# Kernel tuning notes

Measured on AMD Instinct MI355X. Metric: run time of the kernel, lower is better.

Reference implementation:

```python
import jax, jax.numpy as jnp
import numpy as np

START_TAG = 0
END_TAG = 63
NEG_INF = -10000.0


def setup_inputs() -> dict:
    key = jax.random.key(0)
    k1, k2, k3 = jax.random.split(key, 3)
    S, D, L = 32768, 1024, 64  # seq_len, feature_dim, num_labels
    feats = jax.random.normal(k1, (S, D), jnp.float32)
    W = jax.random.normal(k2, (L, D), jnp.float32) * 0.02  # nn.Linear weight [out,in]
    b = jnp.zeros((L,), jnp.float32)
    transitions = jax.random.normal(k3, (L, L), jnp.float32)
    transitions = transitions.at[START_TAG, :].set(NEG_INF).at[:, END_TAG].set(NEG_INF)
    return {"feats": feats, "W": W, "b": b, "transitions": transitions}


def reference(feats, W, b, transitions):
    # emissions: [S, L]
    emissions = feats @ W.T + b

    # Viterbi forward pass.  scores[j] after step t = best path score ending in label j.
    init_scores = transitions[:, START_TAG] + emissions[0]

    def step(scores, emit):
        # swt[j, i] = scores[i] + T[j, i]  (transition i -> j)
        swt = scores[None, :] + transitions  # [L, L]
        new_scores = emit + jnp.max(swt, axis=-1)
        back_ptr = jnp.argmax(swt, axis=-1)
        return new_scores, back_ptr

    final_scores, back_ptrs = jax.lax.scan(step, init_scores, emissions[1:])
    final_scores = final_scores + transitions[END_TAG]

    viterbi_score = jnp.max(final_scores)
    last_tag = jnp.argmax(final_scores)

    # Backtrack: tag[t-1] = back_ptrs[t-1][tag[t]] (back_ptrs[k] is for time k+1).
    def back(tag, bp):
        return bp[tag], tag

    first_tag, rest_tags = jax.lax.scan(back, last_tag, back_ptrs, reverse=True)
    tag_seq = jnp.concatenate([first_tag[None], rest_tags])  # [S]
    return viterbi_score, tag_seq
```

## Files before the change

kernel.cpp:

```cpp
#include <hip/hip_runtime.h>

#define S_LEN 32768
#define D_DIM 1024
#define L_LAB 64
#define LC 32
#define NCH (S_LEN / LC)
#define H_WARM 32
#define CHUNK 128
#define NCHUNK (S_LEN / CHUNK)

#define EM_OFF   0
#define SC_OFF   (S_LEN * 64 * 4)
#define BP_OFF   (SC_OFF + S_LEN * 64 * 4)
#define MAPS_OFF (BP_OFF + S_LEN * 64)
#define BND_OFF  (MAPS_OFF + NCHUNK * 64)
#define WIN_OFF  (BND_OFF + 256)
#define WBF_OFF  (WIN_OFF + NCH * 4)

typedef __attribute__((ext_vector_type(8))) short short8;
typedef __attribute__((ext_vector_type(4))) float floatx4;

__device__ inline unsigned short f32_bf16_rne(float f) {
    unsigned v = __float_as_uint(f);
    v += 0x7FFFu + ((v >> 16) & 1u);
    return (unsigned short)(v >> 16);
}

__global__ __launch_bounds__(256) void wconv_kernel(
        const float* __restrict__ W, unsigned short* __restrict__ Wbf) {
    int i = blockIdx.x * 256 + threadIdx.x;
    Wbf[i] = f32_bf16_rne(W[i]);
}

__global__ __launch_bounds__(256) __attribute__((amdgpu_waves_per_eu(2, 2)))
void emis_kernel(
        const float* __restrict__ feats, const unsigned short* __restrict__ Wbf,
        const float* __restrict__ bvec, float* __restrict__ em) {
    __shared__ __align__(16) unsigned short As[64 * 72];
    __shared__ __align__(16) unsigned short Bs[64 * 72];

    const int tid = threadIdx.x;
    const int lan = tid & 15;
    const int q   = (tid >> 4) & 3;
    const int w   = tid >> 6;
    const int row0 = blockIdx.x * 64;

    floatx4 acc[4];
#pragma unroll
    for (int nt = 0; nt < 4; ++nt) acc[nt] = (floatx4){0.f, 0.f, 0.f, 0.f};

    for (int kb = 0; kb < D_DIM; kb += 64) {
        __syncthreads();
#pragma unroll
        for (int i = 0; i < 4; ++i) {
            int gi = tid + i * 256;
            int m = gi >> 4, g = gi & 15;
            float4 v = *(const float4*)&feats[(size_t)(row0 + m) * D_DIM + kb + g * 4];
            unsigned h0 = f32_bf16_rne(v.x) | ((unsigned)f32_bf16_rne(v.y) << 16);
            unsigned h1 = f32_bf16_rne(v.z) | ((unsigned)f32_bf16_rne(v.w) << 16);
            *(uint2*)&As[m * 72 + g * 4] = (uint2){h0, h1};
        }
#pragma unroll
        for (int i = 0; i < 2; ++i) {
            int gi = tid + i * 256;
            int m = gi >> 3, g = gi & 7;
            *(uint4*)&Bs[m * 72 + g * 8] =
                *(const uint4*)&Wbf[(size_t)m * D_DIM + kb + g * 8];
        }
        __syncthreads();

#pragma unroll
        for (int cc = 0; cc < 2; ++cc) {
            int koff = cc * 32 + q * 8;
            int m_loc = w * 16 + lan;
            short8 av = *(const short8*)&As[m_loc * 72 + koff];
#pragma unroll
            for (int nt = 0; nt < 4; ++nt) {
                int label = nt * 16 + lan;
                short8 bv = *(const short8*)&Bs[label * 72 + koff];
                acc[nt] = __builtin_amdgcn_mfma_f32_16x16x32_bf16(av, bv, acc[nt], 0, 0, 0);
            }
        }
    }

#pragma unroll
    for (int nt = 0; nt < 4; ++nt) {
        int label = nt * 16 + lan;
        float bias = bvec[label];
#pragma unroll
        for (int r = 0; r < 4; ++r) {
            int row = row0 + w * 16 + q * 4 + r;
            em[(size_t)row * 64 + label] = acc[nt][r] + bias;
        }
    }
}

__global__ __launch_bounds__(64) __attribute__((amdgpu_waves_per_eu(1, 1)))
void fwd_chunks(
        const float* __restrict__ em, const float* __restrict__ T,
        float* __restrict__ sc_hist, float* __restrict__ win) {
    const int j = threadIdx.x;
    const int c = blockIdx.x;
    const int a = c * LC;
    const int bend = a + LC;

    float Trow[64];
#pragma unroll
    for (int i = 0; i < 16; ++i)
        ((float4*)Trow)[i] = ((const float4*)(T + j * 64))[i];

    int t0 = a - 1 - H_WARM;
    if (t0 < 0) t0 = 0;

    float sc;
    if (t0 == 0) {
        sc = Trow[0] + em[j];
        if (c == 0) sc_hist[j] = sc;
    } else {
        sc = em[(size_t)t0 * 64 + j];
    }

    auto step = [&](float e) {
        float v[16];
#pragma unroll
        for (int k = 0; k < 16; ++k) {
            float a0 = __int_as_float(__builtin_amdgcn_readlane(__float_as_int(sc), k)) + Trow[k];
            float a1 = __int_as_float(__builtin_amdgcn_readlane(__float_as_int(sc), k + 16)) + Trow[k + 16];
            float a2 = __int_as_float(__builtin_amdgcn_readlane(__float_as_int(sc), k + 32)) + Trow[k + 32];
            float a3 = __int_as_float(__builtin_amdgcn_readlane(__float_as_int(sc), k + 48)) + Trow[k + 48];
            v[k] = fmaxf(fmaxf(fmaxf(a0, a1), a2), a3);
        }
        float r0 = fmaxf(fmaxf(v[0], v[1]), v[2]);
        float r1 = fmaxf(fmaxf(v[3], v[4]), v[5]);
        float r2 = fmaxf(fmaxf(v[6], v[7]), v[8]);
        float r3 = fmaxf(fmaxf(v[9], v[10]), v[11]);
        float r4 = fmaxf(fmaxf(v[12], v[13]), v[14]);
        float s0 = fmaxf(fmaxf(r0, r1), r2);
        float s1 = fmaxf(fmaxf(r3, r4), v[15]);
        sc = e + fmaxf(s0, s1);
    };

    int t = t0 + 1;
    if (t < a) {
        float p0 = em[(size_t)(t + 0) * 64 + j];
        float p1 = em[(size_t)(t + 1) * 64 + j];
        float p2 = em[(size_t)(t + 2) * 64 + j];
        float p3 = em[(size_t)(t + 3) * 64 + j];
        for (; t + 3 < a; t += 4) {
            float n0 = em[(size_t)(t + 4) * 64 + j];
            float n1 = em[(size_t)(t + 5) * 64 + j];
            float n2 = em[(size_t)(t + 6) * 64 + j];
            float n3 = em[(size_t)(t + 7) * 64 + j];
            step(p0); step(p1); step(p2); step(p3);
            p0 = n0; p1 = n1; p2 = n2; p3 = n3;
        }
        for (; t < a; ++t) { step(p0); p0 = p1; p1 = p2; p2 = p3; }
    }
    if (c > 0 && j == 0) win[c] = sc;

    t = (a > 0) ? a : 1;
    {
        float p0 = em[(size_t)(t + 0) * 64 + j];
        float p1 = em[(size_t)(t + 1) * 64 + j];
        float p2 = em[(size_t)(t + 2) * 64 + j];
        float p3 = em[(size_t)(t + 3) * 64 + j];
        for (; t + 3 < bend; t += 4) {
            int t4 = t + 4 > S_LEN - 1 ? S_LEN - 1 : t + 4;
            int t5 = t + 5 > S_LEN - 1 ? S_LEN - 1 : t + 5;
            int t6 = t + 6 > S_LEN - 1 ? S_LEN - 1 : t + 6;
            int t7 = t + 7 > S_LEN - 1 ? S_LEN - 1 : t + 7;
            float n0 = em[(size_t)t4 * 64 + j];
            float n1 = em[(size_t)t5 * 64 + j];
            float n2 = em[(size_t)t6 * 64 + j];
            float n3 = em[(size_t)t7 * 64 + j];
            step(p0); sc_hist[(size_t)(t + 0) * 64 + j] = sc;
            step(p1); sc_hist[(size_t)(t + 1) * 64 + j] = sc;
            step(p2); sc_hist[(size_t)(t + 2) * 64 + j] = sc;
            step(p3); sc_hist[(size_t)(t + 3) * 64 + j] = sc;
            p0 = n0; p1 = n1; p2 = n2; p3 = n3;
        }
        for (; t < bend; ++t) {
            step(p0); sc_hist[(size_t)t * 64 + j] = sc;
            p0 = p1; p1 = p2; p2 = p3;
        }
    }
}

__global__ __launch_bounds__(256) __attribute__((amdgpu_waves_per_eu(2, 2)))
void bp_maps_kernel(
        const float* __restrict__ sc_hist, const float* __restrict__ T,
        unsigned char* __restrict__ bp, unsigned char* __restrict__ maps) {
    __shared__ unsigned char lb[CHUNK * 64];
    const int tid = threadIdx.x;
    const int j = tid & 63;
    const int w = tid >> 6;
    const int c = blockIdx.x;
    const int base = c * CHUNK;

    float Trow[64];
#pragma unroll
    for (int i = 0; i < 16; ++i)
        ((float4*)Trow)[i] = ((const float4*)(T + j * 64))[i];

    for (int k = 0; k < CHUNK / 4; ++k) {
        int tt = w * (CHUNK / 4) + k;
        int t = base + tt;
        int bi = 0;
        if (t >= 1) {
            const float* prev = sc_hist + (size_t)(t - 1) * 64;
            float best = 0.f;
#pragma unroll
            for (int i = 0; i < 64; ++i) {
                float v = prev[i] + Trow[i];
                if (i == 0) best = v;
                else if (v > best) { best = v; bi = i; }
            }
        }
        lb[tt * 64 + j] = (unsigned char)bi;
    }
    __syncthreads();

    uint4* dst = (uint4*)(bp + (size_t)base * 64);
    const uint4* src = (const uint4*)lb;
#pragma unroll
    for (int i = 0; i < 2; ++i) dst[tid + i * 256] = src[tid + i * 256];

    if (tid < 64) {
        int x = tid;
        for (int tt = CHUNK - 1; tt >= 0; --tt) {
            if (base + tt >= 1) x = lb[tt * 64 + x];
        }
        maps[c * 64 + tid] = (unsigned char)x;
    }
}

__global__ __launch_bounds__(256) void finish_kernel(
        const float* __restrict__ sc_hist, const float* __restrict__ T,
        const float* __restrict__ win, const unsigned char* __restrict__ maps,
        float* __restrict__ out, unsigned char* __restrict__ bnd) {
    __shared__ unsigned char lm[NCHUNK * 64];
    __shared__ int lt;
    int tid = threadIdx.x;
    const uint4* src = (const uint4*)maps;
    uint4* dst = (uint4*)lm;
#pragma unroll
    for (int i = 0; i < (NCHUNK * 64 / 16) / 256; ++i) dst[tid + i * 256] = src[tid + i * 256];

    if (tid < 64) {
        int j = tid;
        float part = 0.f;
        for (int c = 1 + j; c < NCH; c += 64) {
            float end_prev = sc_hist[((size_t)c * LC - 1) * 64 + 0];
            part += end_prev - win[c];
        }
#pragma unroll
        for (int off = 32; off; off >>= 1) part += __shfl_xor(part, off, 64);

        float f = sc_hist[(size_t)(S_LEN - 1) * 64 + j] + T[63 * 64 + j];
        float best = 0.f; int bt = 0;
#pragma unroll
        for (int k = 0; k < 64; ++k) {
            float fv = __int_as_float(__builtin_amdgcn_readlane(__float_as_int(f), k));
            if (k == 0) best = fv;
            else if (fv > best) { best = fv; bt = k; }
        }
        if (j == 0) { out[0] = best + part; lt = bt; }
    }
    __syncthreads();
    if (tid == 0) {
        int x = lt;
        bnd[NCHUNK - 1] = (unsigned char)x;
        for (int c = NCHUNK - 1; c >= 1; --c) {
            x = lm[c * 64 + x];
            bnd[c - 1] = (unsigned char)x;
        }
    }
}

__global__ __launch_bounds__(64) void bt_fill(
        const unsigned char* __restrict__ bp, const unsigned char* __restrict__ bnd,
        float* __restrict__ out) {
    __shared__ unsigned char lb[CHUNK * 64];
    int c = blockIdx.x, l = threadIdx.x;
    const uint4* src = (const uint4*)(bp + (size_t)c * CHUNK * 64);
    uint4* dst = (uint4*)lb;
#pragma unroll
    for (int i = 0; i < (CHUNK * 64 / 16) / 64; ++i) dst[l + i * 64] = src[l + i * 64];
    __syncthreads();
    if (l == 0) {
        int t0 = c * CHUNK;
        int x = bnd[c];
        out[1 + t0 + CHUNK - 1] = (float)x;
        for (int tt = CHUNK - 1; tt >= 0; --tt) {
            int t = t0 + tt;
            if (t >= 1) {
                x = lb[tt * 64 + x];
                out[1 + t - 1] = (float)x;
            }
        }
    }
}

extern "C" void kernel_launch(void* const* d_in, const int* in_sizes, int n_in,
                              void* d_out, int out_size, void* d_ws, size_t ws_size,
                              hipStream_t stream) {
    const float* feats = (const float*)d_in[0];
    const float* W     = (const float*)d_in[1];
    const float* b     = (const float*)d_in[2];
    const float* T     = (const float*)d_in[3];
    float* out = (float*)d_out;

    char* ws = (char*)d_ws;
    float*          em       = (float*)(ws + EM_OFF);
    float*          sc_hist  = (float*)(ws + SC_OFF);
    unsigned char*  bp       = (unsigned char*)(ws + BP_OFF);
    unsigned char*  maps     = (unsigned char*)(ws + MAPS_OFF);
    unsigned char*  bnd      = (unsigned char*)(ws + BND_OFF);
    float*          win      = (float*)(ws + WIN_OFF);
    unsigned short* Wbf      = (unsigned short*)(ws + WBF_OFF);

    wconv_kernel<<<(L_LAB * D_DIM) / 256, 256, 0, stream>>>(W, Wbf);
    emis_kernel<<<S_LEN / 64, 256, 0, stream>>>(feats, Wbf, b, em);
    fwd_chunks<<<NCH, 64, 0, stream>>>(em, T, sc_hist, win);
    bp_maps_kernel<<<NCHUNK, 256, 0, stream>>>(sc_hist, T, bp, maps);
    finish_kernel<<<1, 256, 0, stream>>>(sc_hist, T, win, maps, out, bnd);
    bt_fill<<<NCHUNK, 64, 0, stream>>>(bp, bnd, out);
}
```

Baseline: 306.5 us.

## Halve warmup length, pack argmax keys, and hierarchically compose chunk maps

Cuts the chunked-Viterbi warm-up horizon from 32 to 16 steps, which shortens the redundant forward recomputation per chunk. It replaces the compare-and-branch argmax in the backpointer kernel with integer max over packed keys: a bias keeps the scores positive and the low 6 bits hold the reversed index, so ties resolve to the lowest index. The finish kernel now composes chunk maps into super-chunk maps in parallel, so the serial backtrack walks 16 steps instead of 256. The bias and low-bit masking change precision and tie-breaking, and a shorter warm-up risks wrong results if the chunk paths have not yet converged.

```diff
diff --git a/kernel.cpp b/kernel.cpp
--- a/kernel.cpp
+++ b/kernel.cpp
@@ -5,9 +5,11 @@
 #define L_LAB 64
 #define LC 32
 #define NCH (S_LEN / LC)
-#define H_WARM 32
+#define H_WARM 16
 #define CHUNK 128
 #define NCHUNK (S_LEN / CHUNK)
+#define SUP 16
+#define NSUP (NCHUNK / SUP)
 
 #define EM_OFF   0
 #define SC_OFF   (S_LEN * 64 * 4)
@@ -201,6 +203,8 @@
 #pragma unroll
     for (int i = 0; i < 16; ++i)
         ((float4*)Trow)[i] = ((const float4*)(T + j * 64))[i];
+#pragma unroll
+    for (int i = 0; i < 64; ++i) Trow[i] += 32768.0f;
 
     for (int k = 0; k < CHUNK / 4; ++k) {
         int tt = w * (CHUNK / 4) + k;
@@ -208,13 +212,18 @@
         int bi = 0;
         if (t >= 1) {
             const float* prev = sc_hist + (size_t)(t - 1) * 64;
-            float best = 0.f;
-#pragma unroll
-            for (int i = 0; i < 64; ++i) {
-                float v = prev[i] + Trow[i];
-                if (i == 0) best = v;
-                else if (v > best) { best = v; bi = i; }
+            int m0 = 0, m1 = 0, m2 = 0, m3 = 0;
+#pragma unroll
+            for (int i = 0; i < 64; i += 4) {
+                int k0 = (__float_as_int(prev[i + 0] + Trow[i + 0]) & ~63) | (63 - (i + 0));
+                int k1 = (__float_as_int(prev[i + 1] + Trow[i + 1]) & ~63) | (63 - (i + 1));
+                int k2 = (__float_as_int(prev[i + 2] + Trow[i + 2]) & ~63) | (63 - (i + 2));
+                int k3 = (__float_as_int(prev[i + 3] + Trow[i + 3]) & ~63) | (63 - (i + 3));
+                m0 = max(m0, k0); m1 = max(m1, k1);
+                m2 = max(m2, k2); m3 = max(m3, k3);
             }
+            int mm = max(max(m0, m1), max(m2, m3));
+            bi = 63 - (mm & 63);
         }
         lb[tt * 64 + j] = (unsigned char)bi;
     }
@@ -234,17 +243,30 @@
     }
 }
 
-__global__ __launch_bounds__(256) void finish_kernel(
+__global__ __launch_bounds__(512) void finish_kernel(
         const float* __restrict__ sc_hist, const float* __restrict__ T,
         const float* __restrict__ win, const unsigned char* __restrict__ maps,
         float* __restrict__ out, unsigned char* __restrict__ bnd) {
     __shared__ unsigned char lm[NCHUNK * 64];
+    __shared__ unsigned char sm[NSUP * 64];
+    __shared__ unsigned char sb[NSUP];
     __shared__ int lt;
     int tid = threadIdx.x;
     const uint4* src = (const uint4*)maps;
     uint4* dst = (uint4*)lm;
 #pragma unroll
-    for (int i = 0; i < (NCHUNK * 64 / 16) / 256; ++i) dst[tid + i * 256] = src[tid + i * 256];
+    for (int i = 0; i < (NCHUNK * 64 / 16) / 512; ++i) dst[tid + i * 512] = src[tid + i * 512];
+    __syncthreads();
+
+#pragma unroll
+    for (int r = 0; r < 2; ++r) {
+        int idx = tid + r * 512;
+        int s = idx >> 6, jj = idx & 63;
+        int x = jj;
+        for (int q = SUP - 1; q >= 0; --q)
+            x = lm[(s * SUP + q) * 64 + x];
+        sm[s * 64 + jj] = (unsigned char)x;
+    }
 
     if (tid < 64) {
         int j = tid;
@@ -267,12 +289,24 @@
         if (j == 0) { out[0] = best + part; lt = bt; }
     }
     __syncthreads();
+
     if (tid == 0) {
         int x = lt;
-        bnd[NCHUNK - 1] = (unsigned char)x;
-        for (int c = NCHUNK - 1; c >= 1; --c) {
-            x = lm[c * 64 + x];
-            bnd[c - 1] = (unsigned char)x;
+        sb[NSUP - 1] = (unsigned char)x;
+        for (int s = NSUP - 1; s >= 1; --s) {
+            x = sm[s * 64 + x];
+            sb[s - 1] = (unsigned char)x;
+        }
+    }
+    __syncthreads();
+
+    if (tid < NSUP) {
+        int s = tid;
+        int x = sb[s];
+        bnd[s * SUP + SUP - 1] = (unsigned char)x;
+        for (int q = SUP - 1; q >= 1; --q) {
+            x = lm[(s * SUP + q) * 64 + x];
+            bnd[s * SUP + q - 1] = (unsigned char)x;
         }
     }
 }
@@ -323,6 +357,6 @@
     emis_kernel<<<S_LEN / 64, 256, 0, stream>>>(feats, Wbf, b, em);
     fwd_chunks<<<NCH, 64, 0, stream>>>(em, T, sc_hist, win);
     bp_maps_kernel<<<NCHUNK, 256, 0, stream>>>(sc_hist, T, bp, maps);
-    finish_kernel<<<1, 256, 0, stream>>>(sc_hist, T, win, maps, out, bnd);
+    finish_kernel<<<1, 512, 0, stream>>>(sc_hist, T, win, maps, out, bnd);
     bt_fill<<<NCHUNK, 64, 0, stream>>>(bp, bnd, out);
 }
```

After: 278.1 us. 1.1x faster.
